# Optimization experiments

Hardware: AMD Instinct MI355X
Metric: run time of the kernel (lower is better)

The kernel has to match this reference:

```python
import jax, jax.numpy as jnp
import numpy as np

KSIZE = 7
HEAD_DIM = 64
EPS = 1e-6

def rmsnorm(x, w):
    return x * jax.lax.rsqrt(jnp.mean(x * x, axis=-1, keepdims=True) + EPS) * w

def rope2d(x):
    # Split channels: first half rotated by row position, second half by column position.
    B, H, W, C = x.shape
    half = C // 2
    q = half // 2
    inv = 1.0 / (10000.0 ** (jnp.arange(q, dtype=jnp.float32) / q))
    th_y = jnp.arange(H, dtype=jnp.float32)[:, None] * inv  # [H,q]
    th_x = jnp.arange(W, dtype=jnp.float32)[:, None] * inv  # [W,q]
    def rot(v, th):  # v: [...,q,2], th broadcastable to [...,q]
        c, s = jnp.cos(th), jnp.sin(th)
        a, b = v[..., 0], v[..., 1]
        return jnp.stack([a * c - b * s, a * s + b * c], axis=-1)
    xy = rot(x[..., :half].reshape(B, H, W, q, 2), th_y[None, :, None, :])
    xx = rot(x[..., half:].reshape(B, H, W, q, 2), th_x[None, None, :, :])
    return jnp.concatenate([xy.reshape(B, H, W, half), xx.reshape(B, H, W, half)], axis=-1)

def neighborhood_attn(x, w_qkv, w_proj, b_proj, k=KSIZE, hd=HEAD_DIM):
    # NATTEN semantics: each query attends to a k x k window; window start is
    # clamped at borders so every query sees exactly k*k keys.
    B, H, W, C = x.shape
    nh = C // hd
    qkv = x @ w_qkv                           # [B,H,W,3C]
    qv, kv, vv = jnp.split(qkv, 3, axis=-1)
    qh = qv.reshape(B, H, W, nh, hd)
    kh = kv.reshape(B, H, W, nh, hd)
    vh = vv.reshape(B, H, W, nh, hd)
    idx_h = jnp.clip(jnp.arange(H) - k // 2, 0, H - k)[:, None] + jnp.arange(k)  # [H,k]
    idx_w = jnp.clip(jnp.arange(W) - k // 2, 0, W - k)[:, None] + jnp.arange(k)  # [W,k]
    def gather(t):  # [B,H,W,nh,hd] -> [B,H,W,nh,k*k,hd]
        g = t[:, idx_h]            # [B,H,k,W,nh,hd]
        g = g[:, :, :, idx_w]      # [B,H,k,W,k,nh,hd]
        return g.transpose(0, 1, 3, 5, 2, 4, 6).reshape(B, H, W, nh, k * k, hd)
    kn = gather(kh)
    vn = gather(vh)
    scale = 1.0 / np.sqrt(hd).astype(np.float32)
    logits = jnp.einsum('bxynd,bxynkd->bxynk', qh, kn) * scale
    attn = jax.nn.softmax(logits, axis=-1)
    out = jnp.einsum('bxynk,bxynkd->bxynd', attn, vn).reshape(B, H, W, C)
    return out @ w_proj + b_proj

def geglu(x, ff1_w, ff1_b, ff2_w, ff2_b):
    h = x @ ff1_w + ff1_b
    gate, value = jnp.split(h, 2, axis=-1)
    return (jax.nn.gelu(gate, approximate=False) * value) @ ff2_w + ff2_b

def setup_inputs():
    key = jax.random.key(0)
    B, H, W, C = 2, 64, 64, 256
    ks = jax.random.split(key, 8)
    g = lambda k, shape, sc: jax.random.normal(k, shape, jnp.float32) * sc
    return {
        'x': g(ks[0], (B, H, W, C), 1.0),
        'norm1_w': jnp.ones((C,), jnp.float32),
        'norm2_w': jnp.ones((C,), jnp.float32),
        'w_qkv': g(ks[1], (C, 3 * C), 0.02),
        'w_proj': g(ks[2], (C, C), 0.02),
        'b_proj': g(ks[3], (C,), 0.02),
        'ff1_w': g(ks[4], (C, 2 * C), 0.02),
        'ff1_b': g(ks[5], (2 * C,), 0.02),
        'ff2_w': g(ks[6], (C, C), 0.02),
        'ff2_b': g(ks[7], (C,), 0.02),
    }

def reference(x, norm1_w, norm2_w, w_qkv, w_proj, b_proj, ff1_w, ff1_b, ff2_w, ff2_b):
    h = rope2d(rmsnorm(x, norm1_w))
    x = x + neighborhood_attn(h, w_qkv, w_proj, b_proj)
    x = x + geglu(rmsnorm(x, norm2_w), ff1_w, ff1_b, ff2_w, ff2_b)
    return x
```

## Files before the change

kernel.cpp:

```cpp
#include <hip/hip_runtime.h>
#include <hip/hip_bf16.h>


#define ROWS 8192
typedef unsigned int uint32;
typedef unsigned short ushort16;
typedef __attribute__((ext_vector_type(8))) short short8;
typedef __attribute__((ext_vector_type(4))) float floatx4;

__device__ __forceinline__ float bf2f(__hip_bfloat16 b) { return __bfloat162float(b); }
__device__ __forceinline__ float us2f(ushort16 u) {
    return __uint_as_float(((uint32)u) << 16);
}
__device__ __forceinline__ ushort16 f2us(float f) {
    __hip_bfloat16 h = __float2bfloat16(f);
    return *(ushort16*)&h;
}
__device__ __forceinline__ float ldflag(const void* p, size_t i, int f32) {
    return f32 ? ((const float*)p)[i] : bf2f(((const __hip_bfloat16*)p)[i]);
}

__device__ __forceinline__ void gl_lds16(const void* gptr, void* lptr) {
    __builtin_amdgcn_global_load_lds(
        (const __attribute__((address_space(1))) uint32*)gptr,
        (__attribute__((address_space(3))) uint32*)lptr, 16, 0, 0);
}

__global__ __launch_bounds__(64) void detect_kernel(const ushort16* __restrict__ xu,
                                                    int* __restrict__ flag) {
    const int lane = threadIdx.x;
    const float v = us2f(xu[lane * 62]);
    const float a = fabsf(v);
    const bool sane = (a < 1e4f) && (a > 1e-8f);
    const unsigned long long m = __ballot(sane);
    if (lane == 0) flag[0] = (__popcll(m) < 32) ? 1 : 0;
}

struct WSrc {
    const void *wqkv, *wproj, *ff1w, *ff2w, *bproj, *ff1b, *ff2b;
};
__global__ __launch_bounds__(256) void cvt_kernel(WSrc s, ushort16* __restrict__ wT,
                                                  float* __restrict__ bF,
                                                  const int* __restrict__ flag) {
    const int i = blockIdx.x * 256 + threadIdx.x;
    const int f32 = flag[0];
    if (i < 458752) {
        const void* src; int N, base;
        if (i < 196608)      { src = s.wqkv; N = 768; base = 0; }
        else if (i < 262144) { src = s.wproj; N = 256; base = 196608; }
        else if (i < 393216) { src = s.ff1w; N = 512; base = 262144; }
        else                 { src = s.ff2w; N = 256; base = 393216; }
        const int loc = i - base, n = loc >> 8, k = loc & 255;
        wT[i] = f2us(ldflag(src, (size_t)k * N + n, f32));
    } else if (i < 458752 + 1024) {
        const int j = i - 458752;
        float v;
        if (j < 256)      v = ldflag(s.bproj, j, f32);
        else if (j < 768) v = ldflag(s.ff1b, j - 256, f32);
        else              v = ldflag(s.ff2b, j - 768, f32);
        bF[j] = v;
    }
}

template <bool ROPE, bool IN_EXT>
__global__ __launch_bounds__(256) void rmsnorm_kernel(const void* __restrict__ in,
                                                      const void* __restrict__ w,
                                                      ushort16* __restrict__ out,
                                                      const int* __restrict__ flag) {
    const int f32 = flag[0];
    const int row = blockIdx.x;
    const int c = threadIdx.x;
    const size_t idx = (size_t)row * 256 + c;
    float v = IN_EXT ? ldflag(in, idx, f32) : ((const float*)in)[idx];

    float s = v * v;
    #pragma unroll
    for (int off = 32; off; off >>= 1) s += __shfl_xor(s, off);
    __shared__ float red[4];
    if ((c & 63) == 0) red[c >> 6] = s;
    __syncthreads();
    const float sum = red[0] + red[1] + red[2] + red[3];
    const float r = rsqrtf(sum * (1.0f / 256.0f) + 1e-6f);

    float nv = v * r * ldflag(w, c, f32);

    if (ROPE) {
        const int py = (row >> 6) & 63;
        const int px = row & 63;
        const float pos = (c < 128) ? (float)py : (float)px;
        const int j = (c & 127) >> 1;
        const float inv = expf(-(float)j * (9.210340371976184f / 64.0f));
        const float th = pos * inv;
        const float cs = cosf(th), sn = sinf(th);
        const float partner = __shfl_xor(nv, 1);
        nv = ((c & 1) == 0) ? (nv * cs - partner * sn) : (partner * sn + nv * cs);
    }
    out[idx] = f2us(nv);
}

template <int BM, int BN, int WR, int WC, int EPI>
__global__ __launch_bounds__(256) void gemm_mfma(const ushort16* __restrict__ A,
                                                 const ushort16* __restrict__ Bt,
                                                 const float* __restrict__ bias,
                                                 const void* __restrict__ resid,
                                                 void* __restrict__ Cout,
                                                 int N, const int* __restrict__ flag) {
    constexpr int TM = BM / (WR * 16), TN = BN / (WC * 16);
    constexpr int CHA = BM / 16, CHT = (BM + BN) / 16;
    __shared__ ushort16 At[BM * 32];
    __shared__ ushort16 Bs[BN * 32];

    const int f32 = flag[0];
    const int tid = threadIdx.x, lane = tid & 63, wid = tid >> 6;
    const int wr = wid / WC, wc = wid % WC;
    const int m0 = blockIdx.y * BM, n0 = blockIdx.x * BN;
    const int mw = wr * TM * 16, nw = wc * TN * 16;
    const int cr = lane >> 2, cc = (lane & 3) * 8;
    const int l15 = lane & 15, kq = (lane >> 4) * 8;

    floatx4 acc[TM][TN] = {};

    for (int k0 = 0; k0 < 256; k0 += 32) {
        #pragma unroll
        for (int c = 0; c < CHT / 4 + 1; ++c) {
            const int ch = wid + c * 4;
            if (ch < CHT) {
                const ushort16* g;
                ushort16* l;
                if (ch < CHA) {
                    g = A + (size_t)(m0 + ch * 16 + cr) * 256 + k0 + cc;
                    l = At + ch * 512;
                } else {
                    const int c2 = ch - CHA;
                    g = Bt + (size_t)(n0 + c2 * 16 + cr) * 256 + k0 + cc;
                    l = Bs + c2 * 512;
                }
                gl_lds16(g, l);
            }
        }
        __syncthreads();

        short8 af[TM], bf[TN];
        #pragma unroll
        for (int mi = 0; mi < TM; ++mi)
            af[mi] = *(const short8*)&At[(mw + mi * 16 + l15) * 32 + kq];
        #pragma unroll
        for (int nj = 0; nj < TN; ++nj)
            bf[nj] = *(const short8*)&Bs[(nw + nj * 16 + l15) * 32 + kq];
        #pragma unroll
        for (int mi = 0; mi < TM; ++mi)
            #pragma unroll
            for (int nj = 0; nj < TN; ++nj)
                acc[mi][nj] = __builtin_amdgcn_mfma_f32_16x16x32_bf16(af[mi], bf[nj], acc[mi][nj], 0, 0, 0);
        __syncthreads();
    }

    const int crow = (lane >> 4) * 4;
    #pragma unroll
    for (int mi = 0; mi < TM; ++mi) {
        #pragma unroll
        for (int nj = 0; nj < TN; ++nj) {
            const int n = n0 + nw + nj * 16 + l15;
            const float bs = (EPI > 0) ? bias[n] : 0.0f;
            #pragma unroll
            for (int r = 0; r < 4; ++r) {
                const int m = m0 + mw + mi * 16 + crow + r;
                const size_t oi = (size_t)m * N + n;
                float v = acc[mi][nj][r] + bs;
                if (EPI == 1) v += ldflag(resid, oi, f32);
                if (EPI == 3) v += ((const float*)resid)[oi];
                if (EPI == 0 || EPI == 2) {
                    ((ushort16*)Cout)[oi] = f2us(v);
                } else if (EPI == 1) {
                    ((float*)Cout)[oi] = v;
                } else {
                    if (f32) ((float*)Cout)[oi] = v;
                    else     ((ushort16*)Cout)[oi] = f2us(v);
                }
            }
        }
    }
}

__global__ __launch_bounds__(256) void attn_kernel(const ushort16* __restrict__ qkv,
                                                   ushort16* __restrict__ ao) {
    __shared__ ushort16 smem[40208];
    ushort16* const KS = smem;
    ushort16* const VT = smem + 12544;
    ushort16* const PL = smem + 26880;

    const int tid = threadIdx.x, lane = tid & 63, wid = tid >> 6;
    const int l15 = lane & 15, kq8 = (lane >> 4) * 8;
    const int bid = blockIdx.x;
    const int h = bid & 3;
    const int t = (bid >> 2) & 63;
    const int b = bid >> 8;
    const int ty0 = (t >> 3) * 8, tx0 = (t & 7) * 8;
    const int hby = min(max(ty0 - 3, 0), 50);
    const int hbx = min(max(tx0 - 3, 0), 50);
    const int hcol = h * 64;

    const int qpl = wid * 16 + l15;
    const int qpy = ty0 + (qpl >> 3), qpx = tx0 + (qpl & 7);
    const size_t qoff = (size_t)(b * 4096 + qpy * 64 + qpx) * 768 + hcol + kq8;
    const short8 af0 = *(const short8*)&qkv[qoff];
    const short8 af1 = *(const short8*)&qkv[qoff + 32];

    for (int it = tid; it < 3136; it += 256) {
        const bool isK = it < 1568;
        const int task = isK ? it : it - 1568;
        const int key = task >> 3, oct = task & 7;
        const int pix = b * 4096 + (hby + key / 14) * 64 + hbx + key % 14;
        const uint4 d = *(const uint4*)&qkv[(size_t)pix * 768 + (isK ? 256 : 512) + hcol + oct * 8];
        if (isK) {
            uint32* dst = (uint32*)&KS[(oct >> 2) * 6272 + key * 32 + (oct & 3) * 8];
            dst[0] = d.x; dst[1] = d.y; dst[2] = d.z; dst[3] = d.w;
        } else {
            const ushort16* s8 = (const ushort16*)&d;
            #pragma unroll
            for (int j = 0; j < 8; ++j) VT[(oct * 8 + j) * 224 + key] = s8[j];
        }
    }
    for (int it = tid; it < 1792; it += 256)
        VT[(it / 28) * 224 + 196 + (it % 28)] = 0;
    __syncthreads();

    floatx4 acc[13];
    #pragma unroll
    for (int nt = 0; nt < 13; ++nt) {
        const int krow = (nt * 16 + l15) * 32 + kq8;
        const short8 bf0 = *(const short8*)&KS[krow];
        const short8 bf1 = *(const short8*)&KS[6272 + krow];
        floatx4 a = {0.0f, 0.0f, 0.0f, 0.0f};
        a = __builtin_amdgcn_mfma_f32_16x16x32_bf16(af0, bf0, a, 0, 0, 0);
        a = __builtin_amdgcn_mfma_f32_16x16x32_bf16(af1, bf1, a, 0, 0, 0);
        acc[nt] = a;
    }

    int kyA[13], kxA[13];
    #pragma unroll
    for (int nt = 0; nt < 13; ++nt) {
        const int kidx = nt * 16 + l15;
        kyA[nt] = hby + kidx / 14;
        kxA[nt] = hbx + kidx % 14;
    }

    const int crow = (lane >> 4) * 4;
    float rs[4];
    #pragma unroll
    for (int r = 0; r < 4; ++r) {
        const int pl = wid * 16 + crow + r;
        const int py = ty0 + (pl >> 3), px = tx0 + (pl & 7);
        const int sy = min(max(py - 3, 0), 57), sx = min(max(px - 3, 0), 57);
        float lv[13];
        float mx = -1e30f;
        #pragma unroll
        for (int nt = 0; nt < 13; ++nt) {
            const int kidx = nt * 16 + l15;
            const bool valid = (kidx < 196) &&
                               ((unsigned)(kyA[nt] - sy) < 7u) &&
                               ((unsigned)(kxA[nt] - sx) < 7u);
            lv[nt] = valid ? acc[nt][r] * 0.125f : -1e30f;
            mx = fmaxf(mx, lv[nt]);
        }
        #pragma unroll
        for (int off = 1; off < 16; off <<= 1) mx = fmaxf(mx, __shfl_xor(mx, off));
        float sme = 0.0f;
        #pragma unroll
        for (int nt = 0; nt < 13; ++nt) {
            const float e = exp2f((lv[nt] - mx) * 1.4426950408889634f);
            lv[nt] = e;
            sme += e;
        }
        #pragma unroll
        for (int off = 1; off < 16; off <<= 1) sme += __shfl_xor(sme, off);
        rs[r] = 1.0f / sme;
        #pragma unroll
        for (int nt = 0; nt < 13; ++nt)
            PL[pl * 208 + nt * 16 + l15] = f2us(lv[nt]);
    }
    __syncthreads();

    floatx4 oacc[4] = {};
    #pragma unroll
    for (int kc = 0; kc < 7; ++kc) {
        const short8 af = *(const short8*)&PL[(wid * 16 + l15) * 208 + kc * 32 + kq8];
        #pragma unroll
        for (int nd = 0; nd < 4; ++nd) {
            const short8 bf = *(const short8*)&VT[(nd * 16 + l15) * 224 + kc * 32 + kq8];
            oacc[nd] = __builtin_amdgcn_mfma_f32_16x16x32_bf16(af, bf, oacc[nd], 0, 0, 0);
        }
    }
    #pragma unroll
    for (int r = 0; r < 4; ++r) {
        const int pl = wid * 16 + crow + r;
        const int py = ty0 + (pl >> 3), px = tx0 + (pl & 7);
        const size_t o = (size_t)(b * 4096 + py * 64 + px) * 256 + hcol;
        #pragma unroll
        for (int nd = 0; nd < 4; ++nd)
            ao[o + nd * 16 + l15] = f2us(oacc[nd][r] * rs[r]);
    }
}

__global__ __launch_bounds__(256) void geglu_kernel(const ushort16* __restrict__ ffh,
                                                    ushort16* __restrict__ g) {
    const int i = blockIdx.x * 256 + threadIdx.x;
    const int row = i >> 8, c = i & 255;
    const float gate = us2f(ffh[(size_t)row * 512 + c]);
    const float val = us2f(ffh[(size_t)row * 512 + 256 + c]);
    const float ge = 0.5f * gate * (1.0f + erff(gate * 0.70710678118654752f));
    g[i] = f2us(ge * val);
}

extern "C" void kernel_launch(void* const* d_in, const int* in_sizes, int n_in,
                              void* d_out, int out_size, void* d_ws, size_t ws_size,
                              hipStream_t stream) {
    const void* x    = d_in[0];
    const void* n1w  = d_in[1];
    const void* n2w  = d_in[2];
    WSrc ws_src{d_in[3], d_in[4], d_in[6], d_in[8], d_in[5], d_in[7], d_in[9]};

    char* ws = (char*)d_ws;
    int*      flag  = (int*)ws;
    ushort16* wT    = (ushort16*)(ws + 4096);
    float*    bF    = (float*)(ws + 4096 + 458752 * 2);
    ushort16* h     = (ushort16*)(ws + (1 << 20));
    ushort16* qkv   = (ushort16*)(ws + (5 << 20));
    ushort16* ao    = (ushort16*)(ws + (size_t)(17 << 20));
    float*    x1    = (float*)(ws + (size_t)(21 << 20));

    ushort16* wqkvT = wT;
    ushort16* wprojT = wT + 196608;
    ushort16* ff1wT = wT + 262144;
    ushort16* ff2wT = wT + 393216;

    detect_kernel<<<1, 64, 0, stream>>>((const ushort16*)x, flag);
    cvt_kernel<<<1796, 256, 0, stream>>>(ws_src, wT, bF, flag);
    rmsnorm_kernel<true, true><<<ROWS, 256, 0, stream>>>(x, n1w, h, flag);
    gemm_mfma<128, 128, 2, 2, 0><<<dim3(6, 64), 256, 0, stream>>>(h, wqkvT, nullptr, nullptr, qkv, 768, flag);
    attn_kernel<<<512, 256, 0, stream>>>(qkv, ao);
    gemm_mfma<64, 128, 1, 4, 1><<<dim3(2, 128), 256, 0, stream>>>(ao, wprojT, bF, x, x1, 256, flag);
    rmsnorm_kernel<false, false><<<ROWS, 256, 0, stream>>>(x1, n2w, h, flag);
    gemm_mfma<128, 128, 2, 2, 2><<<dim3(4, 64), 256, 0, stream>>>(h, ff1wT, bF + 256, nullptr, qkv, 512, flag);
    geglu_kernel<<<ROWS, 256, 0, stream>>>(qkv, ao);
    gemm_mfma<64, 128, 1, 4, 3><<<dim3(2, 128), 256, 0, stream>>>(ao, ff2wT, bF + 768, x1, d_out, 256, flag);
}
```

Before: 163.2 us.

## Fuse proj GEMM with residual+RMSNorm and FF1 GEMM with GEGLU; tile weight transpose

The projection GEMM now computes full 256-wide rows per block, so it can add the bias and residual, reduce the row sum of squares and emit both x1 and the normalized bf16 input for the FFN. The FF1 GEMM computes gate and value tiles side by side and applies GEGLU in the epilogue, which removes the 512-wide intermediate and the separate geglu kernel. The weight-conversion kernel uses an LDS-tiled transpose for coalesced reads and writes, and the first RMSNorm+RoPE is vectorized to four elements per lane with one row per wavefront. Two launches and an intermediate round trip go away, at the cost of a narrow 32-row proj tile with only 256 blocks.

```diff
diff --git a/kernel.cpp b/kernel.cpp
--- a/kernel.cpp
+++ b/kernel.cpp
@@ -42,60 +42,85 @@
 __global__ __launch_bounds__(256) void cvt_kernel(WSrc s, ushort16* __restrict__ wT,
                                                   float* __restrict__ bF,
                                                   const int* __restrict__ flag) {
-    const int i = blockIdx.x * 256 + threadIdx.x;
     const int f32 = flag[0];
-    if (i < 458752) {
-        const void* src; int N, base;
-        if (i < 196608)      { src = s.wqkv; N = 768; base = 0; }
-        else if (i < 262144) { src = s.wproj; N = 256; base = 196608; }
-        else if (i < 393216) { src = s.ff1w; N = 512; base = 262144; }
-        else                 { src = s.ff2w; N = 256; base = 393216; }
-        const int loc = i - base, n = loc >> 8, k = loc & 255;
-        wT[i] = f2us(ldflag(src, (size_t)k * N + n, f32));
-    } else if (i < 458752 + 1024) {
-        const int j = i - 458752;
-        float v;
-        if (j < 256)      v = ldflag(s.bproj, j, f32);
-        else if (j < 768) v = ldflag(s.ff1b, j - 256, f32);
-        else              v = ldflag(s.ff2b, j - 768, f32);
-        bF[j] = v;
-    }
-}
-
-template <bool ROPE, bool IN_EXT>
-__global__ __launch_bounds__(256) void rmsnorm_kernel(const void* __restrict__ in,
-                                                      const void* __restrict__ w,
-                                                      ushort16* __restrict__ out,
-                                                      const int* __restrict__ flag) {
+    const int bid = blockIdx.x, tid = threadIdx.x;
+    if (bid == 112) {
+        #pragma unroll
+        for (int it = 0; it < 4; ++it) {
+            const int j = it * 256 + tid;
+            float v;
+            if (j < 256)      v = ldflag(s.bproj, j, f32);
+            else if (j < 768) v = ldflag(s.ff1b, j - 256, f32);
+            else              v = ldflag(s.ff2b, j - 768, f32);
+            bF[j] = v;
+        }
+        return;
+    }
+    const void* src; int N, kt, nt, base;
+    if (bid < 48)      { src = s.wqkv;  N = 768; kt = bid / 12;      nt = bid % 12;      base = 0; }
+    else if (bid < 64) { const int l = bid - 48; src = s.wproj; N = 256; kt = l / 4; nt = l % 4; base = 196608; }
+    else if (bid < 96) { const int l = bid - 64; src = s.ff1w;  N = 512; kt = l / 8; nt = l % 8; base = 262144; }
+    else               { const int l = bid - 96; src = s.ff2w;  N = 256; kt = l / 4; nt = l % 4; base = 393216; }
+
+    __shared__ ushort16 T[64][65];
+    const int r0 = tid >> 6, c = tid & 63;
+    #pragma unroll
+    for (int j = 0; j < 16; ++j) {
+        const int r = j * 4 + r0;
+        T[r][c] = f2us(ldflag(src, (size_t)(kt * 64 + r) * N + nt * 64 + c, f32));
+    }
+    __syncthreads();
+    const int n = tid >> 2, kg = tid & 3;
+    #pragma unroll
+    for (int j = 0; j < 16; ++j) {
+        const int k = kg * 16 + j;
+        wT[base + (size_t)(nt * 64 + n) * 256 + kt * 64 + k] = T[k][n];
+    }
+}
+
+__global__ __launch_bounds__(256) void rms1_kernel(const void* __restrict__ in,
+                                                   const void* __restrict__ w,
+                                                   ushort16* __restrict__ out,
+                                                   const int* __restrict__ flag) {
     const int f32 = flag[0];
-    const int row = blockIdx.x;
-    const int c = threadIdx.x;
-    const size_t idx = (size_t)row * 256 + c;
-    float v = IN_EXT ? ldflag(in, idx, f32) : ((const float*)in)[idx];
-
-    float s = v * v;
-    #pragma unroll
-    for (int off = 32; off; off >>= 1) s += __shfl_xor(s, off);
-    __shared__ float red[4];
-    if ((c & 63) == 0) red[c >> 6] = s;
-    __syncthreads();
-    const float sum = red[0] + red[1] + red[2] + red[3];
-    const float r = rsqrtf(sum * (1.0f / 256.0f) + 1e-6f);
-
-    float nv = v * r * ldflag(w, c, f32);
-
-    if (ROPE) {
-        const int py = (row >> 6) & 63;
-        const int px = row & 63;
-        const float pos = (c < 128) ? (float)py : (float)px;
-        const int j = (c & 127) >> 1;
-        const float inv = expf(-(float)j * (9.210340371976184f / 64.0f));
+    const int wid = threadIdx.x >> 6, lane = threadIdx.x & 63;
+    const int row = blockIdx.x * 4 + wid;
+    const int c0 = lane * 4;
+    const size_t base = (size_t)row * 256 + c0;
+
+    float v[4];
+    if (f32) {
+        const float4 d = *(const float4*)((const float*)in + base);
+        v[0] = d.x; v[1] = d.y; v[2] = d.z; v[3] = d.w;
+    } else {
+        const ushort4 d = *(const ushort4*)((const ushort16*)in + base);
+        v[0] = us2f(d.x); v[1] = us2f(d.y); v[2] = us2f(d.z); v[3] = us2f(d.w);
+    }
+
+    float sq = v[0] * v[0] + v[1] * v[1] + v[2] * v[2] + v[3] * v[3];
+    #pragma unroll
+    for (int off = 32; off; off >>= 1) sq += __shfl_xor(sq, off);
+    const float rr = rsqrtf(sq * (1.0f / 256.0f) + 1e-6f);
+
+    float nv[4];
+    #pragma unroll
+    for (int i = 0; i < 4; ++i) nv[i] = v[i] * rr * ldflag(w, c0 + i, f32);
+
+    const int py = (row >> 6) & 63, px = row & 63;
+    const float pos = (c0 < 128) ? (float)py : (float)px;
+    const int j0 = (c0 & 127) >> 1;
+    #pragma unroll
+    for (int p = 0; p < 2; ++p) {
+        const float inv = expf(-(float)(j0 + p) * (9.210340371976184f / 64.0f));
         const float th = pos * inv;
         const float cs = cosf(th), sn = sinf(th);
-        const float partner = __shfl_xor(nv, 1);
-        nv = ((c & 1) == 0) ? (nv * cs - partner * sn) : (partner * sn + nv * cs);
-    }
-    out[idx] = f2us(nv);
+        const float a = nv[p * 2], b = nv[p * 2 + 1];
+        nv[p * 2]     = a * cs - b * sn;
+        nv[p * 2 + 1] = a * sn + b * cs;
+    }
+    ushort4 o;
+    o.x = f2us(nv[0]); o.y = f2us(nv[1]); o.z = f2us(nv[2]); o.w = f2us(nv[3]);
+    *(ushort4*)(out + base) = o;
 }
 
 template <int BM, int BN, int WR, int WC, int EPI>
@@ -167,16 +192,207 @@
                 const int m = m0 + mw + mi * 16 + crow + r;
                 const size_t oi = (size_t)m * N + n;
                 float v = acc[mi][nj][r] + bs;
-                if (EPI == 1) v += ldflag(resid, oi, f32);
                 if (EPI == 3) v += ((const float*)resid)[oi];
-                if (EPI == 0 || EPI == 2) {
+                if (EPI == 0) {
                     ((ushort16*)Cout)[oi] = f2us(v);
-                } else if (EPI == 1) {
-                    ((float*)Cout)[oi] = v;
                 } else {
                     if (f32) ((float*)Cout)[oi] = v;
                     else     ((ushort16*)Cout)[oi] = f2us(v);
                 }
+            }
+        }
+    }
+}
+
+__global__ __launch_bounds__(256) void gemm_proj_rms(const ushort16* __restrict__ A,
+                                                     const ushort16* __restrict__ Bt,
+                                                     const float* __restrict__ bias,
+                                                     const void* __restrict__ xres,
+                                                     const void* __restrict__ n2w,
+                                                     float* __restrict__ x1,
+                                                     ushort16* __restrict__ y,
+                                                     const int* __restrict__ flag) {
+    constexpr int TM = 2, TN = 4;
+    __shared__ ushort16 At[32 * 32];
+    __shared__ ushort16 Bs[256 * 32];
+    __shared__ float red[4][32];
+
+    const int f32 = flag[0];
+    const int tid = threadIdx.x, lane = tid & 63, wid = tid >> 6;
+    const int m0 = blockIdx.x * 32;
+    const int nw = wid * 64;
+    const int cr = lane >> 2, cc = (lane & 3) * 8;
+    const int l15 = lane & 15, kq = (lane >> 4) * 8;
+
+    floatx4 acc[TM][TN] = {};
+
+    for (int k0 = 0; k0 < 256; k0 += 32) {
+        #pragma unroll
+        for (int c = 0; c < 5; ++c) {
+            const int ch = wid + c * 4;
+            if (ch < 18) {
+                const ushort16* g;
+                ushort16* l;
+                if (ch < 2) {
+                    g = A + (size_t)(m0 + ch * 16 + cr) * 256 + k0 + cc;
+                    l = At + ch * 512;
+                } else {
+                    const int c2 = ch - 2;
+                    g = Bt + (size_t)(c2 * 16 + cr) * 256 + k0 + cc;
+                    l = Bs + c2 * 512;
+                }
+                gl_lds16(g, l);
+            }
+        }
+        __syncthreads();
+
+        short8 af[TM], bf[TN];
+        #pragma unroll
+        for (int mi = 0; mi < TM; ++mi)
+            af[mi] = *(const short8*)&At[(mi * 16 + l15) * 32 + kq];
+        #pragma unroll
+        for (int nj = 0; nj < TN; ++nj)
+            bf[nj] = *(const short8*)&Bs[(nw + nj * 16 + l15) * 32 + kq];
+        #pragma unroll
+        for (int mi = 0; mi < TM; ++mi)
+            #pragma unroll
+            for (int nj = 0; nj < TN; ++nj)
+                acc[mi][nj] = __builtin_amdgcn_mfma_f32_16x16x32_bf16(af[mi], bf[nj], acc[mi][nj], 0, 0, 0);
+        __syncthreads();
+    }
+
+    const int crow = (lane >> 4) * 4;
+    float w2[TN], bsv[TN];
+    #pragma unroll
+    for (int nj = 0; nj < TN; ++nj) {
+        const int n = nw + nj * 16 + l15;
+        w2[nj] = ldflag(n2w, n, f32);
+        bsv[nj] = bias[n];
+    }
+
+    float ps[TM][4] = {};
+    #pragma unroll
+    for (int mi = 0; mi < TM; ++mi)
+        #pragma unroll
+        for (int nj = 0; nj < TN; ++nj)
+            #pragma unroll
+            for (int r = 0; r < 4; ++r) {
+                const int m = m0 + mi * 16 + crow + r;
+                const int n = nw + nj * 16 + l15;
+                float v = acc[mi][nj][r] + bsv[nj] + ldflag(xres, (size_t)m * 256 + n, f32);
+                acc[mi][nj][r] = v;
+                ps[mi][r] += v * v;
+            }
+    #pragma unroll
+    for (int off = 1; off < 16; off <<= 1)
+        #pragma unroll
+        for (int mi = 0; mi < TM; ++mi)
+            #pragma unroll
+            for (int r = 0; r < 4; ++r) ps[mi][r] += __shfl_xor(ps[mi][r], off);
+    if (l15 == 0)
+        #pragma unroll
+        for (int mi = 0; mi < TM; ++mi)
+            #pragma unroll
+            for (int r = 0; r < 4; ++r) red[wid][mi * 16 + crow + r] = ps[mi][r];
+    __syncthreads();
+
+    float rr[TM][4];
+    #pragma unroll
+    for (int mi = 0; mi < TM; ++mi)
+        #pragma unroll
+        for (int r = 0; r < 4; ++r) {
+            const int row = mi * 16 + crow + r;
+            const float s = red[0][row] + red[1][row] + red[2][row] + red[3][row];
+            rr[mi][r] = rsqrtf(s * (1.0f / 256.0f) + 1e-6f);
+        }
+    #pragma unroll
+    for (int mi = 0; mi < TM; ++mi)
+        #pragma unroll
+        for (int nj = 0; nj < TN; ++nj)
+            #pragma unroll
+            for (int r = 0; r < 4; ++r) {
+                const int m = m0 + mi * 16 + crow + r;
+                const int n = nw + nj * 16 + l15;
+                const size_t oi = (size_t)m * 256 + n;
+                const float v = acc[mi][nj][r];
+                x1[oi] = v;
+                y[oi] = f2us(v * rr[mi][r] * w2[nj]);
+            }
+}
+
+__global__ __launch_bounds__(256) void gemm_ff1_geglu(const ushort16* __restrict__ A,
+                                                      const ushort16* __restrict__ Bt,
+                                                      const float* __restrict__ bF,
+                                                      ushort16* __restrict__ g,
+                                                      const int* __restrict__ flag) {
+    constexpr int TM = 2, TN = 4;
+    __shared__ ushort16 At[128 * 32];
+    __shared__ ushort16 Bg[64 * 32];
+    __shared__ ushort16 Bv[64 * 32];
+
+    const int tid = threadIdx.x, lane = tid & 63, wid = tid >> 6;
+    const int m0 = blockIdx.y * 128, ng0 = blockIdx.x * 64;
+    const int mw = wid * 32;
+    const int cr = lane >> 2, cc = (lane & 3) * 8;
+    const int l15 = lane & 15, kq = (lane >> 4) * 8;
+
+    floatx4 accg[TM][TN] = {}, accv[TM][TN] = {};
+
+    for (int k0 = 0; k0 < 256; k0 += 32) {
+        #pragma unroll
+        for (int c = 0; c < 4; ++c) {
+            const int ch = wid + c * 4;
+            const ushort16* gp;
+            ushort16* l;
+            if (ch < 8) {
+                gp = A + (size_t)(m0 + ch * 16 + cr) * 256 + k0 + cc;
+                l = At + ch * 512;
+            } else if (ch < 12) {
+                const int c2 = ch - 8;
+                gp = Bt + (size_t)(ng0 + c2 * 16 + cr) * 256 + k0 + cc;
+                l = Bg + c2 * 512;
+            } else {
+                const int c2 = ch - 12;
+                gp = Bt + (size_t)(ng0 + 256 + c2 * 16 + cr) * 256 + k0 + cc;
+                l = Bv + c2 * 512;
+            }
+            gl_lds16(gp, l);
+        }
+        __syncthreads();
+
+        short8 af[TM], bg[TN], bv[TN];
+        #pragma unroll
+        for (int mi = 0; mi < TM; ++mi)
+            af[mi] = *(const short8*)&At[(mw + mi * 16 + l15) * 32 + kq];
+        #pragma unroll
+        for (int nj = 0; nj < TN; ++nj) {
+            bg[nj] = *(const short8*)&Bg[(nj * 16 + l15) * 32 + kq];
+            bv[nj] = *(const short8*)&Bv[(nj * 16 + l15) * 32 + kq];
+        }
+        #pragma unroll
+        for (int mi = 0; mi < TM; ++mi)
+            #pragma unroll
+            for (int nj = 0; nj < TN; ++nj) {
+                accg[mi][nj] = __builtin_amdgcn_mfma_f32_16x16x32_bf16(af[mi], bg[nj], accg[mi][nj], 0, 0, 0);
+                accv[mi][nj] = __builtin_amdgcn_mfma_f32_16x16x32_bf16(af[mi], bv[nj], accv[mi][nj], 0, 0, 0);
+            }
+        __syncthreads();
+    }
+
+    const int crow = (lane >> 4) * 4;
+    #pragma unroll
+    for (int mi = 0; mi < TM; ++mi) {
+        #pragma unroll
+        for (int nj = 0; nj < TN; ++nj) {
+            const int n = ng0 + nj * 16 + l15;
+            const float bg_ = bF[256 + n], bv_ = bF[512 + n];
+            #pragma unroll
+            for (int r = 0; r < 4; ++r) {
+                const int m = m0 + mw + mi * 16 + crow + r;
+                const float gate = accg[mi][nj][r] + bg_;
+                const float val = accv[mi][nj][r] + bv_;
+                const float ge = 0.5f * gate * (1.0f + erff(gate * 0.70710678118654752f));
+                g[(size_t)m * 256 + n] = f2us(ge * val);
             }
         }
     }
@@ -302,46 +518,34 @@
     }
 }
 
-__global__ __launch_bounds__(256) void geglu_kernel(const ushort16* __restrict__ ffh,
-                                                    ushort16* __restrict__ g) {
-    const int i = blockIdx.x * 256 + threadIdx.x;
-    const int row = i >> 8, c = i & 255;
-    const float gate = us2f(ffh[(size_t)row * 512 + c]);
-    const float val = us2f(ffh[(size_t)row * 512 + 256 + c]);
-    const float ge = 0.5f * gate * (1.0f + erff(gate * 0.70710678118654752f));
-    g[i] = f2us(ge * val);
-}
-
 extern "C" void kernel_launch(void* const* d_in, const int* in_sizes, int n_in,
                               void* d_out, int out_size, void* d_ws, size_t ws_size,
                               hipStream_t stream) {
-    const void* x    = d_in[0];
-    const void* n1w  = d_in[1];
-    const void* n2w  = d_in[2];
+    const void* x   = d_in[0];
+    const void* n1w = d_in[1];
+    const void* n2w = d_in[2];
     WSrc ws_src{d_in[3], d_in[4], d_in[6], d_in[8], d_in[5], d_in[7], d_in[9]};
 
     char* ws = (char*)d_ws;
-    int*      flag  = (int*)ws;
-    ushort16* wT    = (ushort16*)(ws + 4096);
-    float*    bF    = (float*)(ws + 4096 + 458752 * 2);
-    ushort16* h     = (ushort16*)(ws + (1 << 20));
-    ushort16* qkv   = (ushort16*)(ws + (5 << 20));
-    ushort16* ao    = (ushort16*)(ws + (size_t)(17 << 20));
-    float*    x1    = (float*)(ws + (size_t)(21 << 20));
-
-    ushort16* wqkvT = wT;
+    int*      flag = (int*)ws;
+    ushort16* wT   = (ushort16*)(ws + 4096);
+    float*    bF   = (float*)(ws + 4096 + 458752 * 2);
+    ushort16* h    = (ushort16*)(ws + (1 << 20));
+    ushort16* qkv  = (ushort16*)(ws + (5 << 20));
+    ushort16* ao   = (ushort16*)(ws + (size_t)(17 << 20));
+    float*    x1   = (float*)(ws + (size_t)(21 << 20));
+
+    ushort16* wqkvT  = wT;
     ushort16* wprojT = wT + 196608;
-    ushort16* ff1wT = wT + 262144;
-    ushort16* ff2wT = wT + 393216;
+    ushort16* ff1wT  = wT + 262144;
+    ushort16* ff2wT  = wT + 393216;
 
     detect_kernel<<<1, 64, 0, stream>>>((const ushort16*)x, flag);
-    cvt_kernel<<<1796, 256, 0, stream>>>(ws_src, wT, bF, flag);
-    rmsnorm_kernel<true, true><<<ROWS, 256, 0, stream>>>(x, n1w, h, flag);
+    cvt_kernel<<<113, 256, 0, stream>>>(ws_src, wT, bF, flag);
+    rms1_kernel<<<2048, 256, 0, stream>>>(x, n1w, h, flag);
     gemm_mfma<128, 128, 2, 2, 0><<<dim3(6, 64), 256, 0, stream>>>(h, wqkvT, nullptr, nullptr, qkv, 768, flag);
     attn_kernel<<<512, 256, 0, stream>>>(qkv, ao);
-    gemm_mfma<64, 128, 1, 4, 1><<<dim3(2, 128), 256, 0, stream>>>(ao, wprojT, bF, x, x1, 256, flag);
-    rmsnorm_kernel<false, false><<<ROWS, 256, 0, stream>>>(x1, n2w, h, flag);
-    gemm_mfma<128, 128, 2, 2, 2><<<dim3(4, 64), 256, 0, stream>>>(h, ff1wT, bF + 256, nullptr, qkv, 512, flag);
-    geglu_kernel<<<ROWS, 256, 0, stream>>>(qkv, ao);
+    gemm_proj_rms<<<256, 256, 0, stream>>>(ao, wprojT, bF, x, n2w, x1, h, flag);
+    gemm_ff1_geglu<<<dim3(4, 64), 256, 0, stream>>>(h, ff1wT, bF, ao, flag);
     gemm_mfma<64, 128, 1, 4, 3><<<dim3(2, 128), 256, 0, stream>>>(ao, ff2wT, bF + 768, x1, d_out, 256, flag);
 }
```

Measured after the change: 153.6 us. 1.06x faster.
